# Performance work log

Hardware: AMD Instinct MI355X
Metric: run time of the kernel (lower is better)

Reference implementation:

```python
import jax, jax.numpy as jnp
import numpy as np

HEADS = 12


def setup_inputs() -> dict:
    rng = jax.random.key(0)
    ks = jax.random.split(rng, 12)
    B, L, D = 8, 64, 768
    s = 1.0 / np.sqrt(D)  # keep projections well-scaled
    return {
        "key": jax.random.normal(ks[0], (B, L, L, D), jnp.float32),
        "value": jax.random.normal(ks[1], (B, L, L, D), jnp.float32),
        "query": jax.random.normal(ks[2], (B, L, D), jnp.float32),
        "mask": jnp.ones((B, L, L), jnp.float32),
        "Wk": jax.random.normal(ks[3], (D, D), jnp.float32) * s,
        "bk": jax.random.normal(ks[4], (D,), jnp.float32) * 0.01,
        "Wv": jax.random.normal(ks[5], (D, D), jnp.float32) * s,
        "bv": jax.random.normal(ks[6], (D,), jnp.float32) * 0.01,
        "Wq": jax.random.normal(ks[7], (D, D), jnp.float32) * s,
        "bq": jax.random.normal(ks[8], (D,), jnp.float32) * 0.01,
        "Wo": jax.random.normal(ks[9], (D, D), jnp.float32) * s,
        "bo": jax.random.normal(ks[10], (D,), jnp.float32) * 0.01,
    }


def reference(key, value, query, mask, Wk, bk, Wv, bv, Wq, bq, Wo, bo):
    # key/value: [B, L, L, D]; query: [B, L, D]; mask: [B, L, L]
    B, L, _, D = key.shape
    h = HEADS
    d = D // h
    # Projections (torch Linear y = x W^T + b; here W stored transposed so y = x @ W + b)
    Kp = (key @ Wk + bk).reshape(B, L, L, h, d)    # [B, i, j, h, d]
    Vp = (value @ Wv + bv).reshape(B, L, L, h, d)  # [B, i, j, h, d]
    Qp = (query @ Wq + bq).reshape(B, L, h, d)     # [B, i, h, d]
    Qp = Qp / jnp.sqrt(jnp.asarray(d, Qp.dtype))
    # scores[b,h,i,j] = sum_d Q[b,i,h,d] * K[b,i,j,h,d]  (query i attends over its own j-row)
    scores = jnp.einsum('bihd,bijhd->bhij', Qp, Kp)
    # multiplicative mask (as in the original: scores = scores * mask)
    scores = scores * mask[:, None, :, :]
    attn = jax.nn.softmax(scores, axis=-1)
    # dropout is identity at inference
    ctx = jnp.einsum('bhij,bijhd->bihd', attn, Vp).reshape(B, L, D)
    return ctx @ Wo + bo  # [B, L, D]
```

## Files before the change

kernel.cpp:

```cpp
#include <hip/hip_runtime.h>

#define DMODEL 768
#define NHEADS 12
#define RTOT   512
#define BIW    9216

__global__ __launch_bounds__(256) void linear16(
    const float* __restrict__ src, int ars, int scm,
    const float* __restrict__ W, const float* __restrict__ bias,
    float* __restrict__ dst, int drs, float scale)
{
    __shared__ float At[16][64];
    __shared__ float Bt[64][32];
    const int rt = blockIdx.x, ct = blockIdx.y, t = threadIdx.x;
    const int sk = ((ct * 32) >> 6) * scm;
    const int c  = t & 31;
    const int rg = t >> 5;

    const int ar0 = t >> 4,          ak0 = t & 15;
    const int bk0 = t >> 3,          bc0 = (t & 7) * 4;
    const int bk1 = (t + 256) >> 3,  bc1 = ((t + 256) & 7) * 4;

    float4 va0, vb0, vb1;
    auto LD = [&](int kb) {
        va0 = *(const float4*)&src[(size_t)(rt * 16 + ar0) * ars + sk + kb * 64 + ak0 * 4];
        vb0 = *(const float4*)&W[(size_t)(kb * 64 + bk0) * DMODEL + ct * 32 + bc0];
        vb1 = *(const float4*)&W[(size_t)(kb * 64 + bk1) * DMODEL + ct * 32 + bc1];
    };

    LD(0);
    float acc[2] = {0.f, 0.f};

    for (int kb = 0; kb < 12; ++kb) {
        if (kb) __syncthreads();
        *(float4*)&At[ar0][ak0 * 4] = va0;
        *(float4*)&Bt[bk0][bc0] = vb0;
        *(float4*)&Bt[bk1][bc1] = vb1;
        __syncthreads();
        if (kb < 11) LD(kb + 1);
        #pragma unroll
        for (int kq = 0; kq < 16; ++kq) {
            float b0 = Bt[kq * 4 + 0][c], b1 = Bt[kq * 4 + 1][c];
            float b2 = Bt[kq * 4 + 2][c], b3 = Bt[kq * 4 + 3][c];
            #pragma unroll
            for (int i = 0; i < 2; ++i) {
                float4 a = *(const float4*)&At[rg * 2 + i][kq * 4];
                acc[i] += a.x * b0 + a.y * b1 + a.z * b2 + a.w * b3;
            }
        }
    }
    const float bb = bias[ct * 32 + c];
    #pragma unroll
    for (int i = 0; i < 2; ++i)
        dst[(size_t)(rt * 16 + rg * 2 + i) * drs + ct * 32 + c] = (acc[i] + bb) * scale;
}

__global__ __launch_bounds__(256) void u_kernel(
    const float* __restrict__ qp, const float* __restrict__ Wk, const float* __restrict__ bk,
    float* __restrict__ u, float* __restrict__ cvec)
{
    __shared__ float Qt[32][64];
    __shared__ float Bt[64][65];
    const int rt = blockIdx.x, mt = blockIdx.y, h = blockIdx.z, t = threadIdx.x;

    #pragma unroll
    for (int kk = 0; kk < 2; ++kk) {
        int i4 = t + kk * 256;
        int r = i4 >> 4, dq = i4 & 15;
        *(float4*)&Qt[r][dq * 4] =
            *(const float4*)&qp[(size_t)(rt * 32 + r) * DMODEL + h * 64 + dq * 4];
    }
    #pragma unroll
    for (int kk = 0; kk < 4; ++kk) {
        int i4 = t + kk * 256;
        int m = i4 >> 4, dq = i4 & 15;
        float4 v = *(const float4*)&Wk[(size_t)(mt * 64 + m) * DMODEL + h * 64 + dq * 4];
        Bt[m][dq * 4 + 0] = v.x; Bt[m][dq * 4 + 1] = v.y;
        Bt[m][dq * 4 + 2] = v.z; Bt[m][dq * 4 + 3] = v.w;
    }
    __syncthreads();

    const int c = t & 63, rg = t >> 6;
    float acc[8] = {0.f,0.f,0.f,0.f,0.f,0.f,0.f,0.f};
    #pragma unroll
    for (int dq = 0; dq < 16; ++dq) {
        float b0 = Bt[c][dq * 4 + 0], b1 = Bt[c][dq * 4 + 1];
        float b2 = Bt[c][dq * 4 + 2], b3 = Bt[c][dq * 4 + 3];
        #pragma unroll
        for (int i = 0; i < 8; ++i) {
            float4 a = *(const float4*)&Qt[rg * 8 + i][dq * 4];
            acc[i] += a.x * b0 + a.y * b1 + a.z * b2 + a.w * b3;
        }
    }
    #pragma unroll
    for (int i = 0; i < 8; ++i)
        u[(size_t)(rt * 32 + rg * 8 + i) * BIW + h * DMODEL + mt * 64 + c] = acc[i];

    if (mt == 0 && t < 32) {
        float s = 0.f;
        for (int d = 0; d < 64; ++d) s += bk[h * 64 + d] * Qt[t][d];
        cvec[(rt * 32 + t) * NHEADS + h] = s;
    }
}

__global__ __launch_bounds__(512, 2) void attn_core(
    const float* __restrict__ key, const float* __restrict__ value, const float* __restrict__ mask,
    const float* __restrict__ u, const float* __restrict__ cvec, float* __restrict__ w)
{
    __shared__ float u_sh[NHEADS * DMODEL];
    __shared__ float sc[NHEADS][66];

    const int bi   = blockIdx.x;
    const int t    = threadIdx.x;
    const int lane = t & 63;
    const int wv   = t >> 6;
    const size_t kvb = (size_t)bi * 64 * DMODEL;

    #pragma unroll
    for (int kk = 0; kk < 5; ++kk) {
        int idx = (t + kk * 512) * 4;
        if (idx < NHEADS * DMODEL)
            *(float4*)&u_sh[idx] = *(const float4*)&u[(size_t)bi * BIW + idx];
    }
    __syncthreads();

    #pragma unroll
    for (int rb = 0; rb < 2; ++rb) {
        const int j0 = wv * 8 + rb * 4;
        float a[NHEADS][4];
        #pragma unroll
        for (int h = 0; h < NHEADS; ++h)
            #pragma unroll
            for (int r = 0; r < 4; ++r) a[h][r] = 0.f;

        float4 kc[4], kn[4];
        #pragma unroll
        for (int r = 0; r < 4; ++r)
            kc[r] = *(const float4*)&key[kvb + (size_t)(j0 + r) * DMODEL + lane * 4];

        #pragma unroll
        for (int cch = 0; cch < 3; ++cch) {
            if (cch < 2) {
                #pragma unroll
                for (int r = 0; r < 4; ++r)
                    kn[r] = *(const float4*)&key[kvb + (size_t)(j0 + r) * DMODEL + (cch + 1) * 256 + lane * 4];
            }
            #pragma unroll
            for (int h = 0; h < NHEADS; ++h) {
                float4 u4 = *(const float4*)&u_sh[h * DMODEL + cch * 256 + lane * 4];
                #pragma unroll
                for (int r = 0; r < 4; ++r)
                    a[h][r] += kc[r].x * u4.x + kc[r].y * u4.y + kc[r].z * u4.z + kc[r].w * u4.w;
            }
            #pragma unroll
            for (int r = 0; r < 4; ++r) kc[r] = kn[r];
        }

        #pragma unroll
        for (int r = 0; r < 4; ++r) {
            float s6[6];
            #pragma unroll
            for (int i = 0; i < 6; ++i) {
                float lo = a[i][r], hi = a[i + 6][r];
                float tl = __shfl_xor(lo, 32), th = __shfl_xor(hi, 32);
                s6[i] = (lane < 32) ? lo + tl : hi + th;
            }
            float s3[3];
            #pragma unroll
            for (int i = 0; i < 3; ++i) {
                float lo = s6[i], hi = s6[i + 3];
                float tl = __shfl_xor(lo, 16), th = __shfl_xor(hi, 16);
                s3[i] = ((lane & 16) == 0) ? lo + tl : hi + th;
            }
            #pragma unroll
            for (int o = 8; o >= 1; o >>= 1)
                #pragma unroll
                for (int i = 0; i < 3; ++i) s3[i] += __shfl_xor(s3[i], o);
            if ((lane & 15) == 0) {
                const int g = lane >> 4;
                #pragma unroll
                for (int i = 0; i < 3; ++i) sc[g * 3 + i][j0 + r] = s3[i];
            }
        }
    }
    __syncthreads();

    {
        const float mk = mask[bi * 64 + lane];
        #pragma unroll
        for (int hh = 0; hh < 2; ++hh) {
            const int h = wv + hh * 8;
            if (h < NHEADS) {
                float s = (sc[h][lane] + cvec[bi * NHEADS + h]) * mk;
                float mx = s;
                #pragma unroll
                for (int o = 1; o < 64; o <<= 1) mx = fmaxf(mx, __shfl_xor(mx, o));
                float e = __expf(s - mx);
                float sm = e;
                #pragma unroll
                for (int o = 1; o < 64; o <<= 1) sm += __shfl_xor(sm, o);
                sc[h][lane] = e / sm;
            }
        }
    }
    __syncthreads();

    {
        const int hb = t >> 8, mo = t & 255;
        const int jbeg = hb * 32;
        float a3[NHEADS][3];
        #pragma unroll
        for (int h = 0; h < NHEADS; ++h) { a3[h][0] = 0.f; a3[h][1] = 0.f; a3[h][2] = 0.f; }
        const float* vb = value + kvb + mo;
        #pragma unroll 4
        for (int jj = 0; jj < 32; ++jj) {
            const int j = jbeg + jj;
            float v0 = vb[(size_t)j * DMODEL];
            float v1 = vb[(size_t)j * DMODEL + 256];
            float v2 = vb[(size_t)j * DMODEL + 512];
            #pragma unroll
            for (int h = 0; h < NHEADS; ++h) {
                float av = sc[h][j];
                a3[h][0] += av * v0;
                a3[h][1] += av * v1;
                a3[h][2] += av * v2;
            }
        }
        if (hb == 0) {
            #pragma unroll
            for (int h = 0; h < NHEADS; ++h)
                #pragma unroll
                for (int mm = 0; mm < 3; ++mm)
                    u_sh[h * DMODEL + mo + mm * 256] = a3[h][mm];
        }
        __syncthreads();
        if (hb == 1) {
            #pragma unroll
            for (int h = 0; h < NHEADS; ++h)
                #pragma unroll
                for (int mm = 0; mm < 3; ++mm)
                    w[(size_t)bi * BIW + h * DMODEL + mo + mm * 256] =
                        a3[h][mm] + u_sh[h * DMODEL + mo + mm * 256];
        }
    }
}

extern "C" void kernel_launch(void* const* d_in, const int* in_sizes, int n_in,
                              void* d_out, int out_size, void* d_ws, size_t ws_size,
                              hipStream_t stream) {
    const float* key   = (const float*)d_in[0];
    const float* value = (const float*)d_in[1];
    const float* query = (const float*)d_in[2];
    const float* mask  = (const float*)d_in[3];
    const float* Wk    = (const float*)d_in[4];
    const float* bk    = (const float*)d_in[5];
    const float* Wv    = (const float*)d_in[6];
    const float* bv    = (const float*)d_in[7];
    const float* Wq    = (const float*)d_in[8];
    const float* bq    = (const float*)d_in[9];
    const float* Wo    = (const float*)d_in[10];
    const float* bo    = (const float*)d_in[11];
    float* out = (float*)d_out;

    float* wsf    = (float*)d_ws;
    float* qp_ctx = wsf;
    float* u_w    = wsf + (size_t)RTOT * DMODEL;
    float* cvec   = u_w + (size_t)RTOT * BIW;

    linear16<<<dim3(32, 24), 256, 0, stream>>>(query, DMODEL, 0, Wq, bq, qp_ctx, DMODEL, 0.125f);
    u_kernel<<<dim3(16, 12, 12), 256, 0, stream>>>(qp_ctx, Wk, bk, u_w, cvec);
    attn_core<<<512, 512, 0, stream>>>(key, value, mask, u_w, cvec, u_w);
    linear16<<<dim3(32, 24), 256, 0, stream>>>(u_w, BIW, DMODEL, Wv, bv, qp_ctx, DMODEL, 1.0f);
    linear16<<<dim3(32, 24), 256, 0, stream>>>(qp_ctx, DMODEL, 0, Wo, bo, out, DMODEL, 1.0f);
}
```

Measured before the change: 154.3 us.

## Double attn_core block to 1024 threads and split heads across waves

Raises the attention-core block from 512 to 1024 threads. Each of the 16 waves now handles 4 key rows in the score phase, and one wave per head does the softmax. In the value phase each thread group covers three heads over all 64 rows, which removes the two-half reduction through shared memory and an extra barrier. The goal is more parallelism and latency hiding per block. In exchange, each thread reads value rows redundantly across four head groups, and the larger per-block footprint can limit occupancy.

```diff
diff --git a/kernel.cpp b/kernel.cpp
--- a/kernel.cpp
+++ b/kernel.cpp
@@ -103,7 +103,7 @@
     }
 }
 
-__global__ __launch_bounds__(512, 2) void attn_core(
+__global__ __launch_bounds__(1024, 4) void attn_core(
     const float* __restrict__ key, const float* __restrict__ value, const float* __restrict__ mask,
     const float* __restrict__ u, const float* __restrict__ cvec, float* __restrict__ w)
 {
@@ -117,16 +117,14 @@
     const size_t kvb = (size_t)bi * 64 * DMODEL;
 
     #pragma unroll
-    for (int kk = 0; kk < 5; ++kk) {
-        int idx = (t + kk * 512) * 4;
-        if (idx < NHEADS * DMODEL)
-            *(float4*)&u_sh[idx] = *(const float4*)&u[(size_t)bi * BIW + idx];
-    }
-    __syncthreads();
-
-    #pragma unroll
-    for (int rb = 0; rb < 2; ++rb) {
-        const int j0 = wv * 8 + rb * 4;
+    for (int kk = 0; kk < 9; ++kk) {
+        int idx = (t + kk * 1024) * 4;
+        *(float4*)&u_sh[idx] = *(const float4*)&u[(size_t)bi * BIW + idx];
+    }
+    __syncthreads();
+
+    {
+        const int j0 = wv * 4;
         float a[NHEADS][4];
         #pragma unroll
         for (int h = 0; h < NHEADS; ++h)
@@ -185,63 +183,46 @@
     }
     __syncthreads();
 
+    if (wv < NHEADS) {
+        const int h = wv;
+        const float mk = mask[bi * 64 + lane];
+        float s = (sc[h][lane] + cvec[bi * NHEADS + h]) * mk;
+        float mx = s;
+        #pragma unroll
+        for (int o = 1; o < 64; o <<= 1) mx = fmaxf(mx, __shfl_xor(mx, o));
+        float e = __expf(s - mx);
+        float sm = e;
+        #pragma unroll
+        for (int o = 1; o < 64; o <<= 1) sm += __shfl_xor(sm, o);
+        sc[h][lane] = e / sm;
+    }
+    __syncthreads();
+
     {
-        const float mk = mask[bi * 64 + lane];
-        #pragma unroll
-        for (int hh = 0; hh < 2; ++hh) {
-            const int h = wv + hh * 8;
-            if (h < NHEADS) {
-                float s = (sc[h][lane] + cvec[bi * NHEADS + h]) * mk;
-                float mx = s;
-                #pragma unroll
-                for (int o = 1; o < 64; o <<= 1) mx = fmaxf(mx, __shfl_xor(mx, o));
-                float e = __expf(s - mx);
-                float sm = e;
-                #pragma unroll
-                for (int o = 1; o < 64; o <<= 1) sm += __shfl_xor(sm, o);
-                sc[h][lane] = e / sm;
-            }
-        }
-    }
-    __syncthreads();
-
-    {
-        const int hb = t >> 8, mo = t & 255;
-        const int jbeg = hb * 32;
-        float a3[NHEADS][3];
-        #pragma unroll
-        for (int h = 0; h < NHEADS; ++h) { a3[h][0] = 0.f; a3[h][1] = 0.f; a3[h][2] = 0.f; }
+        const int hp = t >> 8, mo = t & 255;
+        const int h0 = hp * 3;
+        float a3[3][3];
+        #pragma unroll
+        for (int hh = 0; hh < 3; ++hh) { a3[hh][0] = 0.f; a3[hh][1] = 0.f; a3[hh][2] = 0.f; }
         const float* vb = value + kvb + mo;
         #pragma unroll 4
-        for (int jj = 0; jj < 32; ++jj) {
-            const int j = jbeg + jj;
+        for (int j = 0; j < 64; ++j) {
             float v0 = vb[(size_t)j * DMODEL];
             float v1 = vb[(size_t)j * DMODEL + 256];
             float v2 = vb[(size_t)j * DMODEL + 512];
             #pragma unroll
-            for (int h = 0; h < NHEADS; ++h) {
-                float av = sc[h][j];
-                a3[h][0] += av * v0;
-                a3[h][1] += av * v1;
-                a3[h][2] += av * v2;
-            }
-        }
-        if (hb == 0) {
-            #pragma unroll
-            for (int h = 0; h < NHEADS; ++h)
-                #pragma unroll
-                for (int mm = 0; mm < 3; ++mm)
-                    u_sh[h * DMODEL + mo + mm * 256] = a3[h][mm];
-        }
-        __syncthreads();
-        if (hb == 1) {
-            #pragma unroll
-            for (int h = 0; h < NHEADS; ++h)
-                #pragma unroll
-                for (int mm = 0; mm < 3; ++mm)
-                    w[(size_t)bi * BIW + h * DMODEL + mo + mm * 256] =
-                        a3[h][mm] + u_sh[h * DMODEL + mo + mm * 256];
-        }
+            for (int hh = 0; hh < 3; ++hh) {
+                float av = sc[h0 + hh][j];
+                a3[hh][0] += av * v0;
+                a3[hh][1] += av * v1;
+                a3[hh][2] += av * v2;
+            }
+        }
+        #pragma unroll
+        for (int hh = 0; hh < 3; ++hh)
+            #pragma unroll
+            for (int mm = 0; mm < 3; ++mm)
+                w[(size_t)bi * BIW + (h0 + hh) * DMODEL + mo + mm * 256] = a3[hh][mm];
     }
 }
 
@@ -269,7 +250,7 @@
 
     linear16<<<dim3(32, 24), 256, 0, stream>>>(query, DMODEL, 0, Wq, bq, qp_ctx, DMODEL, 0.125f);
     u_kernel<<<dim3(16, 12, 12), 256, 0, stream>>>(qp_ctx, Wk, bk, u_w, cvec);
-    attn_core<<<512, 512, 0, stream>>>(key, value, mask, u_w, cvec, u_w);
+    attn_core<<<512, 1024, 0, stream>>>(key, value, mask, u_w, cvec, u_w);
     linear16<<<dim3(32, 24), 256, 0, stream>>>(u_w, BIW, DMODEL, Wv, bv, qp_ctx, DMODEL, 1.0f);
     linear16<<<dim3(32, 24), 256, 0, stream>>>(qp_ctx, DMODEL, 0, Wo, bo, out, DMODEL, 1.0f);
 }
```

Result: slower. 259.5 us (+68.1%).
